# Performance work log

Measured on AMD Instinct MI355X. Metric: run time of the kernel, lower is better.

The kernel has to match this reference:

```python
import math
import jax, jax.numpy as jnp
import numpy as np

SHAPES = [(80, 80), (40, 40), (20, 20), (10, 10)]
BS, LQ, D, NH, NL, NP = 8, 1000, 256, 8, 4, 4
C = D // NH


def _offset_bias():
    # replicates _reset_parameters grid_init bias for sampling_offsets
    thetas = np.arange(NH, dtype=np.float32) * (2.0 * math.pi / NH)
    grid = np.stack([np.cos(thetas), np.sin(thetas)], -1)  # [NH,2]
    grid = grid / np.abs(grid).max(-1, keepdims=True)
    grid = np.tile(grid[:, None, None, :], (1, NL, NP, 1))  # [NH,NL,NP,2]
    for i in range(NP):
        grid[:, :, i, :] *= i + 1
    return jnp.asarray(grid.reshape(-1))


def setup_inputs() -> dict:
    key = jax.random.key(0)
    ks = jax.random.split(key, 8)
    len_v = sum(h * w for h, w in SHAPES)
    s = 1.0 / math.sqrt(D)
    starts = np.cumsum([0] + [h * w for h, w in SHAPES])[:-1]
    return {
        "query": jax.random.normal(ks[0], (BS, LQ, D), jnp.float32),
        "reference_points": jax.random.uniform(ks[1], (BS, LQ, NL, 2), jnp.float32),
        "value": jax.random.normal(ks[2], (BS, len_v, D), jnp.float32),
        "w_off": jax.random.normal(ks[3], (D, NH * NL * NP * 2), jnp.float32) * 0.01,
        "b_off": _offset_bias(),
        "w_attn": jax.random.normal(ks[4], (D, NH * NL * NP), jnp.float32) * 0.01,
        "b_attn": jnp.zeros((NH * NL * NP,), jnp.float32),
        "w_v": jax.random.normal(ks[5], (D, D), jnp.float32) * s,
        "b_v": jnp.zeros((D,), jnp.float32),
        "w_o": jax.random.normal(ks[6], (D, D), jnp.float32) * s,
        "b_o": jnp.zeros((D,), jnp.float32),
        "value_spatial_shapes": jnp.array(SHAPES, jnp.int32),
        "value_level_start_index": jnp.array(starts, jnp.int32),
    }


def _sample(img, grid, H, W):
    # bilinear grid_sample, padding_mode='zeros', align_corners=False
    # img: [B, C, H*W], grid: [B, Q, P, 2] in [-1, 1] -> out [B, C, Q, P]
    x = (grid[..., 0] + 1.0) * (W * 0.5) - 0.5
    y = (grid[..., 1] + 1.0) * (H * 0.5) - 0.5
    x0 = jnp.floor(x)
    y0 = jnp.floor(y)
    fx = x - x0
    fy = y - y0
    x0i = x0.astype(jnp.int32)
    y0i = y0.astype(jnp.int32)

    def gather(xi, yi, w):
        valid = (xi >= 0) & (xi < W) & (yi >= 0) & (yi < H)
        idx = jnp.clip(yi, 0, H - 1) * W + jnp.clip(xi, 0, W - 1)
        B, Q, P = idx.shape
        g = jax.vmap(lambda im, ix: im[:, ix])(img, idx.reshape(B, Q * P))  # [B,C,QP]
        return g.reshape(B, -1, Q, P) * (w * valid)[:, None]

    return (gather(x0i, y0i, (1 - fx) * (1 - fy))
            + gather(x0i + 1, y0i, fx * (1 - fy))
            + gather(x0i, y0i + 1, (1 - fx) * fy)
            + gather(x0i + 1, y0i + 1, fx * fy))


def _forward(query, reference_points, value, w_off, b_off, w_attn, b_attn,
             w_v, b_v, w_o, b_o, shapes):
    bs, lq, _ = query.shape
    v = (value @ w_v + b_v).reshape(bs, -1, NH, C)  # [bs, len_v, NH, C]
    off = (query @ w_off + b_off).reshape(bs, lq, NH, NL, NP, 2)
    attn = jax.nn.softmax((query @ w_attn + b_attn).reshape(bs, lq, NH, NL * NP), axis=-1)
    attn = attn.reshape(bs, lq, NH, NL, NP)
    # offset normalizer is spatial_shapes flipped -> (W, H) per level
    norm = jnp.array([[w, h] for h, w in shapes], dtype=query.dtype)  # [NL,2]
    loc = reference_points[:, :, None, :, None, :] + off / norm[None, None, None, :, None, :]
    grids = 2.0 * loc - 1.0  # [bs,lq,NH,NL,NP,2]
    start = 0
    sampled = []
    for lvl, (H, W) in enumerate(shapes):
        v_l = v[:, start:start + H * W].transpose(0, 2, 3, 1).reshape(bs * NH, C, H * W)
        g_l = grids[:, :, :, lvl].transpose(0, 2, 1, 3, 4).reshape(bs * NH, lq, NP, 2)
        sampled.append(_sample(v_l, g_l, H, W))  # [bs*NH, C, lq, NP]
        start += H * W
    samp = jnp.stack(sampled, axis=3).reshape(bs * NH, C, lq, NL * NP)
    aw = attn.transpose(0, 2, 1, 3, 4).reshape(bs * NH, 1, lq, NL * NP)
    out = (samp * aw).sum(-1).reshape(bs, NH * C, lq).transpose(0, 2, 1)  # [bs,lq,D]
    return out @ w_o + b_o


def reference(query, reference_points, value, w_off, b_off, w_attn, b_attn,
              w_v, b_v, w_o, b_o, value_spatial_shapes, value_level_start_index):
    shapes = [tuple(int(x) for x in r) for r in np.asarray(value_spatial_shapes)]
    return _forward(query, reference_points, value, w_off, b_off, w_attn, b_attn,
                    w_v, b_v, w_o, b_o, shapes)
```

## Files before the change

### kernel.cpp

```cpp
#include <hip/hip_runtime.h>
#include <hip/hip_bf16.h>
#include <math.h>

#define BS     8
#define LQ     1000
#define DMODEL 256
#define NH     8
#define NLV    4
#define NPT    4
#define LEN_V  8500
#define NQ     (BS*LQ)
#define MV     (BS*LEN_V)
#define KS     8

typedef __attribute__((ext_vector_type(8))) short short8;
typedef __attribute__((ext_vector_type(4))) float floatx4;

static __device__ __forceinline__ unsigned short f2bf(float f) {
    __hip_bfloat16 h = __float2bfloat16(f);
    return __builtin_bit_cast(unsigned short, h);
}
static __device__ __forceinline__ float asf(unsigned int u) {
    return __builtin_bit_cast(float, u);
}

static __device__ __forceinline__ void dma16(const unsigned short* g, unsigned short* lds) {
    __builtin_amdgcn_global_load_lds(
        (const __attribute__((address_space(1))) unsigned int*)g,
        (__attribute__((address_space(3))) unsigned int*)lds,
        16, 0, 0);
}

template <bool OUT_BF16>
__global__ __launch_bounds__(256, 2) void mfma_gemm_dma(
    const unsigned short* __restrict__ Ab, const unsigned short* __restrict__ Bfrag,
    const float* __restrict__ bias1, const float* __restrict__ bias2, int nsplit,
    void* __restrict__ Cptr, int M)
{
    __shared__ unsigned short As[2][16384];

    const int tid = threadIdx.x;
    const int l   = tid & 63;
    const int w   = tid >> 6;
    const int bn  = blockIdx.y;
    const int lm  = l & 15;
    const int lk  = l >> 4;
    const int x7  = lm & 7;
    const int N   = (int)gridDim.y * 128;
    const int n_mtiles = (M + 63) >> 6;

    short8 Bf[2][KS];
    const int u0 = bn * 8 + w * 2;
    #pragma unroll
    for (int j = 0; j < 2; ++j)
        #pragma unroll
        for (int s = 0; s < KS; ++s)
            Bf[j][s] = *(const short8*)(Bfrag + ((size_t)((u0 + j) * KS + s) * 64 + l) * 8);

    auto dma_tile = [&](int tile, int buf) {
        #pragma unroll
        for (int j = 0; j < 8; ++j) {
            const int slot = j * 256 + tid;
            const int row  = slot >> 5;
            const int gp   = slot & 31;
            const int gc   = gp ^ (row & 7);
            int grow = tile * 64 + row; grow = grow < M ? grow : M - 1;
            dma16(Ab + (size_t)grow * 256 + gc * 8,
                  &As[buf][(j * 256 + w * 64) * 8]);
        }
    };

    int bm  = blockIdx.x;
    int buf = 0;
    if (bm < n_mtiles) dma_tile(bm, 0);

    while (bm < n_mtiles) {
        const int bm_next = bm + (int)gridDim.x;

        __builtin_amdgcn_s_waitcnt(0);
        __syncthreads();
        if (bm_next < n_mtiles) dma_tile(bm_next, buf ^ 1);

        floatx4 acc[4][2];
        #pragma unroll
        for (int i = 0; i < 4; ++i)
            #pragma unroll
            for (int j = 0; j < 2; ++j)
                #pragma unroll
                for (int r = 0; r < 4; ++r) acc[i][j][r] = 0.f;

        #pragma unroll
        for (int s = 0; s < KS; ++s) {
            short8 afr[4];
            #pragma unroll
            for (int i = 0; i < 4; ++i)
                afr[i] = *(const short8*)(
                    &As[buf][(i * 16 + lm) * 256 + (((s * 4 + lk) ^ x7)) * 8]);
            #pragma unroll
            for (int i = 0; i < 4; ++i)
                #pragma unroll
                for (int j = 0; j < 2; ++j)
                    acc[i][j] = __builtin_amdgcn_mfma_f32_16x16x32_bf16(
                                    afr[i], Bf[j][s], acc[i][j], 0, 0, 0);
        }

        #pragma unroll
        for (int j = 0; j < 2; ++j) {
            const int col = bn * 128 + w * 32 + j * 16 + lm;
            const float bv = (bias2 != nullptr && col >= nsplit) ? bias2[col - nsplit]
                                                                 : bias1[col];
            #pragma unroll
            for (int i = 0; i < 4; ++i) {
                const int rbase = bm * 64 + i * 16 + lk * 4;
                #pragma unroll
                for (int r = 0; r < 4; ++r) {
                    const int row = rbase + r;
                    if (row < M) {
                        const float v = acc[i][j][r] + bv;
                        if (OUT_BF16)
                            ((unsigned short*)Cptr)[(size_t)row * N + col] = f2bf(v);
                        else
                            ((float*)Cptr)[(size_t)row * N + col] = v;
                    }
                }
            }
        }

        buf ^= 1;
        bm = bm_next;
    }
}

__global__ __launch_bounds__(256) void wtransform(
    const float* __restrict__ w_v, const float* __restrict__ w_off,
    const float* __restrict__ w_attn, const float* __restrict__ w_o,
    unsigned short* __restrict__ wv_f, unsigned short* __restrict__ woa_f,
    unsigned short* __restrict__ wo_f)
{
    const int gid = blockIdx.x * 256 + threadIdx.x;
    int chunk, mode;
    if (gid < 8192)               { chunk = gid;         mode = 0; }
    else if (gid < 8192 + 12288)  { chunk = gid - 8192;  mode = 1; }
    else                          { chunk = gid - 20480; mode = 2; }
    const int l = chunk & 63, s = (chunk >> 6) & 7, u = chunk >> 9;
    short8 o;
    #pragma unroll
    for (int j = 0; j < 8; ++j) {
        const int k = s * 32 + (l >> 4) * 8 + j;
        const int n = u * 16 + (l & 15);
        float v;
        if (mode == 0)      v = w_v[k * 256 + n];
        else if (mode == 1) v = (n < 256) ? w_off[k * 256 + n] : w_attn[k * 128 + (n - 256)];
        else                v = w_o[k * 256 + n];
        o[j] = (short)f2bf(v);
    }
    unsigned short* dp = (mode == 0 ? wv_f : mode == 1 ? woa_f : wo_f)
                         + ((size_t)(u * 8 + s) * 64 + l) * 8;
    *(short8*)dp = o;
}

__global__ __launch_bounds__(256) void cast2_bf16(const float* __restrict__ value,
                                                  const float* __restrict__ query,
                                                  unsigned short* __restrict__ out)
{
    const int i = blockIdx.x * 256 + threadIdx.x;
    const float4 v = (i < 4352000) ? ((const float4*)value)[i]
                                   : ((const float4*)query)[i - 4352000];
    ushort4 o;
    o.x = f2bf(v.x); o.y = f2bf(v.y); o.z = f2bf(v.z); o.w = f2bf(v.w);
    ((ushort4*)out)[i] = o;
}

__global__ __launch_bounds__(256) void ms_sample_fused(
    const unsigned short* __restrict__ v,
    const float* __restrict__ offattn,
    const float* __restrict__ refp,
    const unsigned short* __restrict__ wo_f,
    const float* __restrict__ b_o,
    float* __restrict__ out)
{
    __shared__ float offx_s[8][16][8];
    __shared__ float offy_s[8][16][8];
    __shared__ float atw_s [8][16][8];
    __shared__ float ref_s [8][8];
    __shared__ unsigned short P[8][256];

    const int tid = threadIdx.x;
    const int bswz = blockIdx.x & 7;
    const int iq0  = bswz * 1000 + (blockIdx.x >> 3) * 8;

    if (tid < 64) {
        const int q = tid >> 3, h = tid & 7;
        const float* rowp = offattn + (size_t)(iq0 + q) * 384;
        float lg[16];
        float m = -1e30f;
        #pragma unroll
        for (int i = 0; i < 16; ++i) { lg[i] = rowp[256 + h * 16 + i]; m = fmaxf(m, lg[i]); }
        float s = 0.f;
        #pragma unroll
        for (int i = 0; i < 16; ++i) { lg[i] = __expf(lg[i] - m); s += lg[i]; }
        const float inv = 1.f / s;
        #pragma unroll
        for (int i = 0; i < 16; ++i) atw_s[q][i][h] = lg[i] * inv;
        #pragma unroll
        for (int i = 0; i < 16; ++i) {
            offx_s[q][i][h] = rowp[(h * 16 + i) * 2 + 0];
            offy_s[q][i][h] = rowp[(h * 16 + i) * 2 + 1];
        }
        if (h == 0) {
            #pragma unroll
            for (int i = 0; i < 8; ++i) ref_s[q][i] = refp[(size_t)(iq0 + q) * 8 + i];
        }
    }
    __syncthreads();

    const int q8  = tid >> 5;
    const int sub = tid & 31;
    const int h   = sub >> 2;
    const int oct = sub & 3;

    float acc[8] = {0.f, 0.f, 0.f, 0.f, 0.f, 0.f, 0.f, 0.f};
    const unsigned short* vb = v + (size_t)bswz * LEN_V * 256 + h * 32 + oct * 8;
    const int Hs[4] = {80, 40, 20, 10};
    const int st[4] = {0, 6400, 8000, 8400};

    #pragma unroll
    for (int lvl = 0; lvl < NLV; ++lvl) {
        const int W = Hs[lvl];
        const float bx = ref_s[q8][lvl * 2 + 0] * (float)W - 0.5f;
        const float by = ref_s[q8][lvl * 2 + 1] * (float)W - 0.5f;
        const unsigned short* vl = vb + (size_t)st[lvl] * 256;
        #pragma unroll
        for (int p = 0; p < NPT; ++p) {
            const int lp = lvl * 4 + p;
            const float x  = bx + offx_s[q8][lp][h];
            const float y  = by + offy_s[q8][lp][h];
            const float at = atw_s[q8][lp][h];
            const float x0f = floorf(x), y0f = floorf(y);
            const float fx = x - x0f, fy = y - y0f;
            const int x0 = (int)x0f, y0 = (int)y0f;
            const int x1 = x0 + 1,   y1 = y0 + 1;
            const int cx0 = min(max(x0, 0), W - 1);
            const int cx1 = min(max(x1, 0), W - 1);
            const int cy0 = min(max(y0, 0), W - 1);
            const int cy1 = min(max(y1, 0), W - 1);
            const float vx0 = (x0 >= 0 && x0 < W) ? 1.f : 0.f;
            const float vx1 = (x1 >= 0 && x1 < W) ? 1.f : 0.f;
            const float vy0 = (y0 >= 0 && y0 < W) ? 1.f : 0.f;
            const float vy1 = (y1 >= 0 && y1 < W) ? 1.f : 0.f;
            const float w00 = at * (1.f - fx) * (1.f - fy) * vx0 * vy0;
            const float w01 = at * fx * (1.f - fy) * vx1 * vy0;
            const float w10 = at * (1.f - fx) * fy * vx0 * vy1;
            const float w11 = at * fx * fy * vx1 * vy1;
            const unsigned short* r0 = vl + (size_t)(cy0 * W) * 256;
            const unsigned short* r1 = vl + (size_t)(cy1 * W) * 256;
            const uint4 d00 = *(const uint4*)(r0 + (size_t)cx0 * 256);
            const uint4 d01 = *(const uint4*)(r0 + (size_t)cx1 * 256);
            const uint4 d10 = *(const uint4*)(r1 + (size_t)cx0 * 256);
            const uint4 d11 = *(const uint4*)(r1 + (size_t)cx1 * 256);
            acc[0] += w00 * asf(d00.x << 16) + w01 * asf(d01.x << 16)
                    + w10 * asf(d10.x << 16) + w11 * asf(d11.x << 16);
            acc[1] += w00 * asf(d00.x & 0xffff0000u) + w01 * asf(d01.x & 0xffff0000u)
                    + w10 * asf(d10.x & 0xffff0000u) + w11 * asf(d11.x & 0xffff0000u);
            acc[2] += w00 * asf(d00.y << 16) + w01 * asf(d01.y << 16)
                    + w10 * asf(d10.y << 16) + w11 * asf(d11.y << 16);
            acc[3] += w00 * asf(d00.y & 0xffff0000u) + w01 * asf(d01.y & 0xffff0000u)
                    + w10 * asf(d10.y & 0xffff0000u) + w11 * asf(d11.y & 0xffff0000u);
            acc[4] += w00 * asf(d00.z << 16) + w01 * asf(d01.z << 16)
                    + w10 * asf(d10.z << 16) + w11 * asf(d11.z << 16);
            acc[5] += w00 * asf(d00.z & 0xffff0000u) + w01 * asf(d01.z & 0xffff0000u)
                    + w10 * asf(d10.z & 0xffff0000u) + w11 * asf(d11.z & 0xffff0000u);
            acc[6] += w00 * asf(d00.w << 16) + w01 * asf(d01.w << 16)
                    + w10 * asf(d10.w << 16) + w11 * asf(d11.w << 16);
            acc[7] += w00 * asf(d00.w & 0xffff0000u) + w01 * asf(d01.w & 0xffff0000u)
                    + w10 * asf(d10.w & 0xffff0000u) + w11 * asf(d11.w & 0xffff0000u);
        }
    }

    {
        short8 o;
        #pragma unroll
        for (int j = 0; j < 8; ++j) o[j] = (short)f2bf(acc[j]);
        *(short8*)(&P[q8][sub * 8]) = o;
    }
    __syncthreads();

    const int l  = tid & 63;
    const int w  = tid >> 6;
    const int lm = l & 15;
    const int lk = l >> 4;

    floatx4 acc2[4];
    #pragma unroll
    for (int jj = 0; jj < 4; ++jj)
        #pragma unroll
        for (int r = 0; r < 4; ++r) acc2[jj][r] = 0.f;

    #pragma unroll
    for (int s = 0; s < KS; ++s) {
        short8 afr;
        if (lm < 8) afr = *(const short8*)(&P[lm][s * 32 + lk * 8]);
        else { short8 z = {0,0,0,0,0,0,0,0}; afr = z; }
        #pragma unroll
        for (int jj = 0; jj < 4; ++jj) {
            const int u = w * 4 + jj;
            short8 bfr = *(const short8*)(wo_f + ((size_t)(u * KS + s) * 64 + l) * 8);
            acc2[jj] = __builtin_amdgcn_mfma_f32_16x16x32_bf16(afr, bfr, acc2[jj], 0, 0, 0);
        }
    }

    if (lk < 2) {
        #pragma unroll
        for (int jj = 0; jj < 4; ++jj) {
            const int col = w * 64 + jj * 16 + lm;
            const float bv = b_o[col];
            #pragma unroll
            for (int r = 0; r < 4; ++r) {
                const int row = lk * 4 + r;
                out[(size_t)(iq0 + row) * 256 + col] = acc2[jj][r] + bv;
            }
        }
    }
}

extern "C" void kernel_launch(void* const* d_in, const int* in_sizes, int n_in,
                              void* d_out, int out_size, void* d_ws, size_t ws_size,
                              hipStream_t stream)
{
    const float* query  = (const float*)d_in[0];
    const float* refp   = (const float*)d_in[1];
    const float* value  = (const float*)d_in[2];
    const float* w_off  = (const float*)d_in[3];
    const float* b_off  = (const float*)d_in[4];
    const float* w_attn = (const float*)d_in[5];
    const float* b_attn = (const float*)d_in[6];
    const float* w_v    = (const float*)d_in[7];
    const float* b_v    = (const float*)d_in[8];
    const float* w_o    = (const float*)d_in[9];
    const float* b_o    = (const float*)d_in[10];
    (void)d_in[11]; (void)d_in[12];

    float* out = (float*)d_out;

    char* ws = (char*)d_ws;
    unsigned short* valq_bf = (unsigned short*)ws;
    unsigned short* v_proj  = (unsigned short*)(ws + 38912000);
    float*          offattn = (float*)(ws + 73728000);
    unsigned short* wv_f    = (unsigned short*)(ws + 86016000);
    unsigned short* woa_f   = (unsigned short*)(ws + 86147072);
    unsigned short* wo_f    = (unsigned short*)(ws + 86343680);

    dim3 blk(256);

    hipLaunchKernelGGL(wtransform, dim3(112), blk, 0, stream,
                       w_v, w_off, w_attn, w_o, wv_f, woa_f, wo_f);
    hipLaunchKernelGGL(cast2_bf16, dim3(19000), blk, 0, stream,
                       value, query, valq_bf);
    hipLaunchKernelGGL((mfma_gemm_dma<true>), dim3(532, 2), blk, 0, stream,
                       valq_bf, wv_f, b_v, nullptr, 1 << 30, v_proj, MV);
    hipLaunchKernelGGL((mfma_gemm_dma<false>), dim3(125, 3), blk, 0, stream,
                       valq_bf + (size_t)MV * 256, woa_f, b_off, b_attn, 256, offattn, NQ);
    hipLaunchKernelGGL(ms_sample_fused, dim3(1000), blk, 0, stream,
                       v_proj, offattn, refp, wo_f, b_o, out);
}
```

Before: 213.2 us.

## Split sampling across levels with 512 threads and move output projection to GEMM

The sampling kernel now runs 512 threads per block, with each half handling two of the four levels, and combines the two partial sums through shared memory. The fused per-block output projection, which wasted half of its MFMA rows on padding, is removed. The pre-projection activations are written as bf16 to the workspace, reusing the value/query buffer, and a separate tiled GEMM launch applies w_o and b_o. This raises parallelism for the gather-bound sampling and gives the projection a full-tile GEMM. The cost is an extra launch and an extra global round trip for the intermediate.

```diff
diff --git a/kernel.cpp b/kernel.cpp
--- a/kernel.cpp
+++ b/kernel.cpp
@@ -171,21 +171,19 @@
     ((ushort4*)out)[i] = o;
 }
 
-__global__ __launch_bounds__(256) void ms_sample_fused(
+__global__ __launch_bounds__(512) void ms_sample_split(
     const unsigned short* __restrict__ v,
     const float* __restrict__ offattn,
     const float* __restrict__ refp,
-    const unsigned short* __restrict__ wo_f,
-    const float* __restrict__ b_o,
-    float* __restrict__ out)
+    unsigned short* __restrict__ out_pre)
 {
     __shared__ float offx_s[8][16][8];
     __shared__ float offy_s[8][16][8];
     __shared__ float atw_s [8][16][8];
     __shared__ float ref_s [8][8];
-    __shared__ unsigned short P[8][256];
-
-    const int tid = threadIdx.x;
+    __shared__ float part  [8][32][9];
+
+    const int tid  = threadIdx.x;
     const int bswz = blockIdx.x & 7;
     const int iq0  = bswz * 1000 + (blockIdx.x >> 3) * 8;
 
@@ -214,10 +212,11 @@
     }
     __syncthreads();
 
-    const int q8  = tid >> 5;
-    const int sub = tid & 31;
-    const int h   = sub >> 2;
-    const int oct = sub & 3;
+    const int q8   = tid >> 6;
+    const int half = (tid >> 5) & 1;
+    const int sub  = tid & 31;
+    const int h    = sub >> 2;
+    const int oct  = sub & 3;
 
     float acc[8] = {0.f, 0.f, 0.f, 0.f, 0.f, 0.f, 0.f, 0.f};
     const unsigned short* vb = v + (size_t)bswz * LEN_V * 256 + h * 32 + oct * 8;
@@ -225,7 +224,8 @@
     const int st[4] = {0, 6400, 8000, 8400};
 
     #pragma unroll
-    for (int lvl = 0; lvl < NLV; ++lvl) {
+    for (int li = 0; li < 2; ++li) {
+        const int lvl = half * 2 + li;
         const int W = Hs[lvl];
         const float bx = ref_s[q8][lvl * 2 + 0] * (float)W - 0.5f;
         const float by = ref_s[q8][lvl * 2 + 1] * (float)W - 0.5f;
@@ -277,49 +277,16 @@
         }
     }
 
-    {
+    if (half == 1) {
+        #pragma unroll
+        for (int j = 0; j < 8; ++j) part[q8][sub][j] = acc[j];
+    }
+    __syncthreads();
+    if (half == 0) {
         short8 o;
         #pragma unroll
-        for (int j = 0; j < 8; ++j) o[j] = (short)f2bf(acc[j]);
-        *(short8*)(&P[q8][sub * 8]) = o;
-    }
-    __syncthreads();
-
-    const int l  = tid & 63;
-    const int w  = tid >> 6;
-    const int lm = l & 15;
-    const int lk = l >> 4;
-
-    floatx4 acc2[4];
-    #pragma unroll
-    for (int jj = 0; jj < 4; ++jj)
-        #pragma unroll
-        for (int r = 0; r < 4; ++r) acc2[jj][r] = 0.f;
-
-    #pragma unroll
-    for (int s = 0; s < KS; ++s) {
-        short8 afr;
-        if (lm < 8) afr = *(const short8*)(&P[lm][s * 32 + lk * 8]);
-        else { short8 z = {0,0,0,0,0,0,0,0}; afr = z; }
-        #pragma unroll
-        for (int jj = 0; jj < 4; ++jj) {
-            const int u = w * 4 + jj;
-            short8 bfr = *(const short8*)(wo_f + ((size_t)(u * KS + s) * 64 + l) * 8);
-            acc2[jj] = __builtin_amdgcn_mfma_f32_16x16x32_bf16(afr, bfr, acc2[jj], 0, 0, 0);
-        }
-    }
-
-    if (lk < 2) {
-        #pragma unroll
-        for (int jj = 0; jj < 4; ++jj) {
-            const int col = w * 64 + jj * 16 + lm;
-            const float bv = b_o[col];
-            #pragma unroll
-            for (int r = 0; r < 4; ++r) {
-                const int row = lk * 4 + r;
-                out[(size_t)(iq0 + row) * 256 + col] = acc2[jj][r] + bv;
-            }
-        }
+        for (int j = 0; j < 8; ++j) o[j] = (short)f2bf(acc[j] + part[q8][sub][j]);
+        *(short8*)(out_pre + (size_t)(iq0 + q8) * 256 + sub * 8) = o;
     }
 }
 
@@ -344,6 +311,7 @@
 
     char* ws = (char*)d_ws;
     unsigned short* valq_bf = (unsigned short*)ws;
+    unsigned short* out_pre = (unsigned short*)ws;
     unsigned short* v_proj  = (unsigned short*)(ws + 38912000);
     float*          offattn = (float*)(ws + 73728000);
     unsigned short* wv_f    = (unsigned short*)(ws + 86016000);
@@ -360,6 +328,8 @@
                        valq_bf, wv_f, b_v, nullptr, 1 << 30, v_proj, MV);
     hipLaunchKernelGGL((mfma_gemm_dma<false>), dim3(125, 3), blk, 0, stream,
                        valq_bf + (size_t)MV * 256, woa_f, b_off, b_attn, 256, offattn, NQ);
-    hipLaunchKernelGGL(ms_sample_fused, dim3(1000), blk, 0, stream,
-                       v_proj, offattn, refp, wo_f, b_o, out);
-}
+    hipLaunchKernelGGL(ms_sample_split, dim3(1000), dim3(512), 0, stream,
+                       v_proj, offattn, refp, out_pre);
+    hipLaunchKernelGGL((mfma_gemm_dma<false>), dim3(125, 2), blk, 0, stream,
+                       out_pre, wo_f, b_o, nullptr, 1 << 30, out, NQ);
+}
```

After: 201.8 us. -5.4%, faster.
